# Performance work log

Measured on AMD Instinct MI355X. Metric: run time of the kernel, lower is better.

The kernel has to match this reference:

```python
import jax, jax.numpy as jnp
import numpy as np

BS, TPD, D = 16384, 4, 128
G, M = 4, 4096


def setup_inputs() -> dict:
    key = jax.random.key(0)
    k1, k2 = jax.random.split(key)
    return {
        "x": jax.random.normal(k1, (BS, TPD, D), dtype=jnp.float32),
        "embeddings": jax.random.normal(k2, (G, M, D), dtype=jnp.float32),
        "count": jnp.zeros((G, M), dtype=jnp.float32),
    }


def reference(x, embeddings, count):
    bs, tpd, d = x.shape
    g, m, _ = embeddings.shape
    # (BS, TPD, D) -> (N, G, D) -> (G, N, D), N = BS*TPD/G
    xg = x.reshape(-1, g, d).transpose(1, 0, 2)
    # squared euclidean distances (argmin identical to cdist argmin)
    x2 = jnp.sum(xg * xg, axis=-1)[:, :, None]            # (G, N, 1)
    e2 = jnp.sum(embeddings * embeddings, axis=-1)[:, None, :]  # (G, 1, M)
    dist = x2 + e2 - 2.0 * jnp.einsum('gnd,gmd->gnm', xg, embeddings)  # (G, N, M)
    indices = jnp.argmin(dist, axis=-1)                   # (G, N) int
    # usage-count scatter add (buffer update in torch forward)
    new_count = count.at[jnp.arange(g)[:, None], indices].add(1.0)
    # gather quantized embeddings: (G, N, D)
    x_quant = embeddings[jnp.arange(g)[:, None], indices]
    x_quant = x_quant.transpose(1, 0, 2).reshape(bs, tpd, d)
    ind_out = indices.transpose(1, 0).reshape(bs, tpd)
    return (x_quant, ind_out, new_count)
```

## Files before the change

kernel.cpp:

```cpp
#include <hip/hip_runtime.h>

#define G 4
#define M 4096
#define D 128
#define NQ 16384
#define NROWS 65536
#define OFF_IND 8388608
#define OFF_CNT (OFF_IND + NROWS)
#define DELTA 0.02f

typedef unsigned int u32;
typedef unsigned short u16;
typedef __attribute__((ext_vector_type(8))) short bf16x8;
typedef __attribute__((ext_vector_type(4))) float f32x4;

__device__ __forceinline__ u16 f2bf(float f) {
    u32 u = __float_as_uint(f);
    u32 r = (u + 0x7FFFu + ((u >> 16) & 1u)) >> 16;
    return (u16)r;
}
__device__ __forceinline__ float bf2f(u16 b) { return __uint_as_float((u32)b << 16); }


__global__ __launch_bounds__(256) void prep_x(const float* __restrict__ x,
                                              u32* __restrict__ xfrag) {
    const int tid = threadIdx.x, lane = tid & 63;
    const int c = blockIdx.x * 4 + (tid >> 6);
    const int ks = c & 3, qt = c >> 2;
    const int qrow = qt * 16 + (lane & 15);
    const int g = qrow >> 14, n = qrow & 16383;
    const int k = ks * 32 + (lane >> 4) * 8;
    const float* src = x + ((size_t)n * 4 + g) * D + k;
    const float4 a = *(const float4*)src;
    const float4 b = *(const float4*)(src + 4);
    const float v[8] = {a.x, a.y, a.z, a.w, b.x, b.y, b.z, b.w};
    u32 hi[4], lo[4];
#pragma unroll
    for (int i = 0; i < 4; ++i) {
        const float v0 = -2.0f * v[2 * i], v1 = -2.0f * v[2 * i + 1];
        const u16 h0 = f2bf(v0), h1 = f2bf(v1);
        const u16 l0 = f2bf(v0 - bf2f(h0)), l1 = f2bf(v1 - bf2f(h1));
        hi[i] = (u32)h0 | ((u32)h1 << 16);
        lo[i] = (u32)l0 | ((u32)l1 << 16);
    }
    const u32 base = (u32)((qt * 4 + ks) * 2) * 256 + lane * 4;
    *(uint4*)(xfrag + base)       = make_uint4(hi[0], hi[1], hi[2], hi[3]);
    *(uint4*)(xfrag + base + 256) = make_uint4(lo[0], lo[1], lo[2], lo[3]);
}

__global__ __launch_bounds__(256) void prep_emb(const float* __restrict__ emb,
                                                u32* __restrict__ efrag) {
    const int tid = threadIdx.x, lane = tid & 63;
    const int c = blockIdx.x * 4 + (tid >> 6);
    const int ks = c & 3, mt = (c >> 2) & 255, g = c >> 10;
    const int m = mt * 16 + (lane & 15);
    const int k = ks * 32 + (lane >> 4) * 8;
    const float* src = emb + ((size_t)g * M + m) * D + k;
    const float4 a = *(const float4*)src;
    const float4 b = *(const float4*)(src + 4);
    const float v[8] = {a.x, a.y, a.z, a.w, b.x, b.y, b.z, b.w};
    u32 hi[4], lo[4];
#pragma unroll
    for (int i = 0; i < 4; ++i) {
        const float v0 = v[2 * i], v1 = v[2 * i + 1];
        const u16 h0 = f2bf(v0), h1 = f2bf(v1);
        const u16 l0 = f2bf(v0 - bf2f(h0)), l1 = f2bf(v1 - bf2f(h1));
        hi[i] = (u32)h0 | ((u32)h1 << 16);
        lo[i] = (u32)l0 | ((u32)l1 << 16);
    }
    const u32 base = (u32)(g * 256 + mt) * 2048 + (u32)(ks * 2) * 256 + lane * 4;
    *(uint4*)(efrag + base)       = make_uint4(hi[0], hi[1], hi[2], hi[3]);
    *(uint4*)(efrag + base + 256) = make_uint4(lo[0], lo[1], lo[2], lo[3]);
}

__global__ __launch_bounds__(256) void e2f_kernel(const float* __restrict__ emb,
                                                  float* __restrict__ e2f) {
    const int row = blockIdx.x * 4 + (threadIdx.x >> 6);
    const int lane = threadIdx.x & 63;
    const float2 v = ((const float2*)(emb + (size_t)row * D))[lane];
    double s = (double)v.x * (double)v.x + (double)v.y * (double)v.y;
#pragma unroll
    for (int off = 1; off < 64; off <<= 1) s += __shfl_xor(s, off, 64);
    if (lane == 0) e2f[row] = (float)s;
}

__global__ __launch_bounds__(256) void vq_mfma(const u32* __restrict__ xfrag,
                                               const u32* __restrict__ efrag,
                                               const float* __restrict__ e2f,
                                               float* __restrict__ out,
                                               int* __restrict__ flagcnt,
                                               int* __restrict__ flaglist) {
    __shared__ float e2s[M];
    __shared__ u32 ebuf[2][2048];

    const int tid = threadIdx.x, w = tid >> 6, lane = tid & 63;
    const int g = blockIdx.x >> 7, qb = blockIdx.x & 127;

    const float* e2g = e2f + (size_t)g * M;
    for (int i = tid; i < M / 4; i += 256) ((float4*)e2s)[i] = ((const float4*)e2g)[i];

    const bf16x8* xp = (const bf16x8*)xfrag;
    const int qt0 = g * 1024 + qb * 8 + w * 2;
    bf16x8 xf[2][4][2];
#pragma unroll
    for (int f = 0; f < 2; ++f)
#pragma unroll
        for (int ks = 0; ks < 4; ++ks)
#pragma unroll
            for (int h = 0; h < 2; ++h)
                xf[f][ks][h] = xp[(size_t)(((qt0 + f) * 4 + ks) * 2 + h) * 64 + lane];

    float b1[8], b2[8];
    int i1[8];
#pragma unroll
    for (int s = 0; s < 8; ++s) { b1[s] = 3.4e38f; b2[s] = 3.4e38f; i1[s] = 0; }

    const uint4* eg = (const uint4*)(efrag + (size_t)g * 256 * 2048);
    {
        const uint4 s0 = eg[tid], s1 = eg[256 + tid];
        ((uint4*)ebuf[0])[tid] = s0;
        ((uint4*)ebuf[0])[256 + tid] = s1;
    }
    __syncthreads();

    int cur = 0;
    for (int mc = 0; mc < 256; ++mc) {
        uint4 s0, s1;
        const bool pf = (mc + 1 < 256);
        if (pf) {
            const uint4* src = eg + (size_t)(mc + 1) * 512;
            s0 = src[tid];
            s1 = src[256 + tid];
        }
        const bf16x8* bp = (const bf16x8*)ebuf[cur];
        bf16x8 bh[4], bl[4];
#pragma unroll
        for (int ks = 0; ks < 4; ++ks) {
            bh[ks] = bp[(ks * 2 + 0) * 64 + lane];
            bl[ks] = bp[(ks * 2 + 1) * 64 + lane];
        }
        f32x4 acc0 = {0.f, 0.f, 0.f, 0.f}, acc1 = {0.f, 0.f, 0.f, 0.f};
#pragma unroll
        for (int ks = 0; ks < 4; ++ks) {
            acc0 = __builtin_amdgcn_mfma_f32_16x16x32_bf16(xf[0][ks][1], bh[ks], acc0, 0, 0, 0);
            acc1 = __builtin_amdgcn_mfma_f32_16x16x32_bf16(xf[1][ks][1], bh[ks], acc1, 0, 0, 0);
        }
#pragma unroll
        for (int ks = 0; ks < 4; ++ks) {
            acc0 = __builtin_amdgcn_mfma_f32_16x16x32_bf16(xf[0][ks][0], bl[ks], acc0, 0, 0, 0);
            acc1 = __builtin_amdgcn_mfma_f32_16x16x32_bf16(xf[1][ks][0], bl[ks], acc1, 0, 0, 0);
        }
#pragma unroll
        for (int ks = 0; ks < 4; ++ks) {
            acc0 = __builtin_amdgcn_mfma_f32_16x16x32_bf16(xf[0][ks][0], bh[ks], acc0, 0, 0, 0);
            acc1 = __builtin_amdgcn_mfma_f32_16x16x32_bf16(xf[1][ks][0], bh[ks], acc1, 0, 0, 0);
        }
        const int mcol = mc * 16 + (lane & 15);
        const float e2m = e2s[mcol];
#pragma unroll
        for (int r = 0; r < 4; ++r) {
            const float s0v = acc0[r] + e2m;
            b2[r] = fminf(b2[r], fmaxf(b1[r], s0v));
            i1[r] = (s0v < b1[r]) ? mcol : i1[r];
            b1[r] = fminf(b1[r], s0v);
            const float s1v = acc1[r] + e2m;
            b2[r + 4] = fminf(b2[r + 4], fmaxf(b1[r + 4], s1v));
            i1[r + 4] = (s1v < b1[r + 4]) ? mcol : i1[r + 4];
            b1[r + 4] = fminf(b1[r + 4], s1v);
        }
        if (pf) {
            uint4* dst = (uint4*)ebuf[cur ^ 1];
            dst[tid] = s0;
            dst[256 + tid] = s1;
        }
        __syncthreads();
        cur ^= 1;
    }

#pragma unroll
    for (int s = 0; s < 8; ++s) {
        float v1 = b1[s], v2 = b2[s];
        int j1 = i1[s];
#pragma unroll
        for (int off = 1; off < 16; off <<= 1) {
            const float o1 = __shfl_xor(v1, off, 64);
            const int   oj = __shfl_xor(j1, off, 64);
            const float o2 = __shfl_xor(v2, off, 64);
            v2 = fminf(fminf(v2, o2), fmaxf(v1, o1));
            if (o1 < v1 || (o1 == v1 && oj < j1)) { v1 = o1; j1 = oj; }
        }
        if ((lane & 15) == 0) {
            const int n = qb * 128 + w * 32 + (s >> 2) * 16 + (lane >> 4) * 4 + (s & 3);
            if (v2 - v1 > DELTA) {
                out[(size_t)OFF_IND + (size_t)n * 4 + g] = (float)j1;
                atomicAdd(out + OFF_CNT + (size_t)g * M + j1, 1.0f);
            } else {
                const int pos = atomicAdd(flagcnt, 1);
                if (pos < NROWS) flaglist[pos] = (g << 14) | n;
            }
        }
    }
}

__global__ __launch_bounds__(256) void recheck(const float* __restrict__ x,
                                               const float* __restrict__ emb,
                                               const int* __restrict__ flagcnt,
                                               const int* __restrict__ flaglist,
                                               float* __restrict__ out) {
    __shared__ float xs[D];
    __shared__ double wv[4];
    __shared__ int wi[4];
    const int tid = threadIdx.x;
    int nf = *flagcnt;
    if (nf > NROWS) nf = NROWS;
    for (int it = blockIdx.x; it < nf; it += gridDim.x) {
        const int qid = flaglist[it];
        const int g = qid >> 14, n = qid & 16383;
        __syncthreads();
        if (tid < 32) ((float4*)xs)[tid] = ((const float4*)(x + ((size_t)n * 4 + g) * D))[tid];
        __syncthreads();
        double best = 1e300;
        int bi = 0;
        for (int j = 0; j < 16; ++j) {
            const int m = tid + j * 256;
            const float* e = emb + ((size_t)g * M + m) * D;
            double dot = 0.0, ee = 0.0;
            for (int k = 0; k < D; k += 4) {
                const float4 ev = *(const float4*)(e + k);
                const double e0 = ev.x, e1 = ev.y, e2v = ev.z, e3 = ev.w;
                dot = fma((double)xs[k + 0], e0, dot);
                dot = fma((double)xs[k + 1], e1, dot);
                dot = fma((double)xs[k + 2], e2v, dot);
                dot = fma((double)xs[k + 3], e3, dot);
                ee = fma(e0, e0, ee); ee = fma(e1, e1, ee);
                ee = fma(e2v, e2v, ee); ee = fma(e3, e3, ee);
            }
            const double s = ee - 2.0 * dot;
            if (s < best) { best = s; bi = m; }
        }
        for (int off = 1; off < 64; off <<= 1) {
            const double ob = __shfl_xor(best, off, 64);
            const int oi = __shfl_xor(bi, off, 64);
            if (ob < best || (ob == best && oi < bi)) { best = ob; bi = oi; }
        }
        if ((tid & 63) == 0) { wv[tid >> 6] = best; wi[tid >> 6] = bi; }
        __syncthreads();
        if (tid == 0) {
            double bv = wv[0];
            int bj = wi[0];
            for (int u = 1; u < 4; ++u)
                if (wv[u] < bv || (wv[u] == bv && wi[u] < bj)) { bv = wv[u]; bj = wi[u]; }
            out[(size_t)OFF_IND + (size_t)n * 4 + g] = (float)bj;
            atomicAdd(out + OFF_CNT + (size_t)g * M + bj, 1.0f);
        }
    }
}

__global__ __launch_bounds__(256) void gather_kernel(const float* __restrict__ emb,
                                                     const float* __restrict__ indf,
                                                     float* __restrict__ xq) {
    const int rid = blockIdx.x * 8 + (threadIdx.x >> 5);
    const int lane = threadIdx.x & 31;
    const int g = rid & 3;
    const int m = (int)indf[rid];
    const float4 v = ((const float4*)(emb + ((size_t)g * M + m) * D))[lane];
    ((float4*)(xq + (size_t)rid * D))[lane] = v;
}


#define QT 64
#define MT 128
#define KT 32
#define XPAD 132
#define EPAD 36

__global__ __launch_bounds__(256) void e2d_kernel(const float* __restrict__ emb,
                                                  double* __restrict__ e2) {
    int row = blockIdx.x * 4 + (threadIdx.x >> 6);
    int lane = threadIdx.x & 63;
    const float2 v = ((const float2*)(emb + (size_t)row * D))[lane];
    double s = (double)v.x * (double)v.x + (double)v.y * (double)v.y;
#pragma unroll
    for (int off = 1; off < 64; off <<= 1) s += __shfl_xor(s, off, 64);
    if (lane == 0) e2[row] = s;
}

__global__ __launch_bounds__(256) void argmin_kernel(const float* __restrict__ x,
                                                     const float* __restrict__ emb,
                                                     const double* __restrict__ e2,
                                                     float* __restrict__ out) {
    __shared__ float xs[QT][XPAD];
    __shared__ float es[MT][EPAD];
    const int g = blockIdx.x >> 8;
    const int n0 = (blockIdx.x & 255) * QT;
    const int tid = threadIdx.x;
    const int tm = tid & 15;
    const int tq = tid >> 4;
#pragma unroll
    for (int it = 0; it < 8; ++it) {
        int idx = it * 256 + tid;
        int r = idx >> 5, c2 = idx & 31;
        const float4 v = ((const float4*)(x + ((size_t)((n0 + r) * 4 + g)) * D))[c2];
        *(float4*)&xs[r][c2 * 4] = v;
    }
    double best[4];
    int bm[4];
#pragma unroll
    for (int qi = 0; qi < 4; ++qi) { best[qi] = 1e300; bm[qi] = 0; }
    const double* e2g = e2 + (size_t)g * M;
    const float* eg = emb + (size_t)g * M * D;
    for (int mc = 0; mc < M / MT; ++mc) {
        const int m0 = mc * MT;
        double acc[4][8];
#pragma unroll
        for (int qi = 0; qi < 4; ++qi)
#pragma unroll
            for (int mi = 0; mi < 8; ++mi) acc[qi][mi] = 0.0;
        for (int kc = 0; kc < D / KT; ++kc) {
            __syncthreads();
#pragma unroll
            for (int it = 0; it < 4; ++it) {
                int idx = it * 256 + tid;
                int r = idx >> 3, c2 = idx & 7;
                const float4 v = ((const float4*)(eg + (size_t)(m0 + r) * D + kc * KT))[c2];
                *(float4*)&es[r][c2 * 4] = v;
            }
            __syncthreads();
#pragma unroll
            for (int kk = 0; kk < KT; kk += 4) {
                double xv[4][4];
#pragma unroll
                for (int qi = 0; qi < 4; ++qi) {
                    const float4 v = *(const float4*)&xs[tq + 16 * qi][kc * KT + kk];
                    xv[qi][0] = v.x; xv[qi][1] = v.y; xv[qi][2] = v.z; xv[qi][3] = v.w;
                }
#pragma unroll
                for (int mi = 0; mi < 8; ++mi) {
                    const float4 v = *(const float4*)&es[tm + 16 * mi][kk];
                    const double e0 = v.x, e1 = v.y, e2v = v.z, e3 = v.w;
#pragma unroll
                    for (int qi = 0; qi < 4; ++qi) {
                        acc[qi][mi] = fma(xv[qi][0], e0, acc[qi][mi]);
                        acc[qi][mi] = fma(xv[qi][1], e1, acc[qi][mi]);
                        acc[qi][mi] = fma(xv[qi][2], e2v, acc[qi][mi]);
                        acc[qi][mi] = fma(xv[qi][3], e3, acc[qi][mi]);
                    }
                }
            }
        }
#pragma unroll
        for (int mi = 0; mi < 8; ++mi) {
            const int m = m0 + tm + 16 * mi;
            const double e2m = e2g[m];
#pragma unroll
            for (int qi = 0; qi < 4; ++qi) {
                const double s = e2m - 2.0 * acc[qi][mi];
                if (s < best[qi]) { best[qi] = s; bm[qi] = m; }
            }
        }
    }
#pragma unroll
    for (int qi = 0; qi < 4; ++qi) {
        double v = best[qi];
        int i = bm[qi];
#pragma unroll
        for (int off = 1; off < 16; off <<= 1) {
            const double ov = __shfl_xor(v, off, 64);
            const int oi = __shfl_xor(i, off, 64);
            if (ov < v || (ov == v && oi < i)) { v = ov; i = oi; }
        }
        if (tm == 0) {
            const int n = n0 + tq + 16 * qi;
            out[(size_t)OFF_IND + (size_t)n * 4 + g] = (float)i;
            atomicAdd(out + OFF_CNT + (size_t)g * M + i, 1.0f);
        }
    }
}


extern "C" void kernel_launch(void* const* d_in, const int* in_sizes, int n_in,
                              void* d_out, int out_size, void* d_ws, size_t ws_size,
                              hipStream_t stream) {
    const float* x   = (const float*)d_in[0];
    const float* emb = (const float*)d_in[1];
    const float* cnt = (const float*)d_in[2];
    float* out = (float*)d_out;

    if (ws_size >= 8716544) {
        u32*   efrag    = (u32*)d_ws;
        float* e2fp     = (float*)((char*)d_ws + 8388608);
        int*   flagcnt  = (int*)((char*)d_ws + 8454144);
        int*   flaglist = (int*)((char*)d_ws + 8454400);
        u32*   xfrag    = (u32*)d_out;

        hipLaunchKernelGGL(prep_x,   dim3(4096), dim3(256), 0, stream, x, xfrag);
        hipLaunchKernelGGL(prep_emb, dim3(1024), dim3(256), 0, stream, emb, efrag);
        hipLaunchKernelGGL(e2f_kernel, dim3(4096), dim3(256), 0, stream, emb, e2fp);
        hipMemcpyAsync(out + OFF_CNT, cnt, (size_t)G * M * sizeof(float),
                       hipMemcpyDeviceToDevice, stream);
        hipMemsetAsync(flagcnt, 0, 4, stream);
        hipLaunchKernelGGL(vq_mfma, dim3(512), dim3(256), 0, stream,
                           xfrag, efrag, e2fp, out, flagcnt, flaglist);
        hipLaunchKernelGGL(recheck, dim3(256), dim3(256), 0, stream,
                           x, emb, flagcnt, flaglist, out);
        hipLaunchKernelGGL(gather_kernel, dim3(NROWS / 8), dim3(256), 0, stream,
                           emb, out + OFF_IND, out);
    } else {
        double* e2 = (double*)d_ws;
        hipLaunchKernelGGL(e2d_kernel, dim3(4096), dim3(256), 0, stream, emb, e2);
        hipMemcpyAsync(out + OFF_CNT, cnt, (size_t)G * M * sizeof(float),
                       hipMemcpyDeviceToDevice, stream);
        hipLaunchKernelGGL(argmin_kernel, dim3((NQ / QT) * G), dim3(256), 0, stream,
                           x, emb, e2, out);
        hipLaunchKernelGGL(gather_kernel, dim3(NROWS / 8), dim3(256), 0, stream,
                           emb, out + OFF_IND, out);
    }
}
```

Baseline: 368.4 us.

## Split codebook across blocks, fuse x prep into MFMA kernel, merge partial argmins

The main distance kernel now splits each group's codebook into two halves, which doubles the grid to 1024 blocks for better CU occupancy. A new merge kernel combines the per-half best and second-best results before the ambiguity check. The x bf16 hi/lo conversion moves into the MFMA kernel, and the embedding-norm computation is fused into the embedding prep kernel with atomics. The e2 bias is folded into the MFMA accumulator init, and the recheck grid is enlarged. This adds partial-result traffic and a launch, and the norms are now accumulated in float instead of double.

```diff
diff --git a/kernel.cpp b/kernel.cpp
--- a/kernel.cpp
+++ b/kernel.cpp
@@ -16,40 +16,16 @@
 
 __device__ __forceinline__ u16 f2bf(float f) {
     u32 u = __float_as_uint(f);
-    u32 r = (u + 0x7FFFu + ((u >> 16) & 1u)) >> 16;
-    return (u16)r;
+    return (u16)((u + 0x7FFFu + ((u >> 16) & 1u)) >> 16);
 }
 __device__ __forceinline__ float bf2f(u16 b) { return __uint_as_float((u32)b << 16); }
 
-
-__global__ __launch_bounds__(256) void prep_x(const float* __restrict__ x,
-                                              u32* __restrict__ xfrag) {
-    const int tid = threadIdx.x, lane = tid & 63;
-    const int c = blockIdx.x * 4 + (tid >> 6);
-    const int ks = c & 3, qt = c >> 2;
-    const int qrow = qt * 16 + (lane & 15);
-    const int g = qrow >> 14, n = qrow & 16383;
-    const int k = ks * 32 + (lane >> 4) * 8;
-    const float* src = x + ((size_t)n * 4 + g) * D + k;
-    const float4 a = *(const float4*)src;
-    const float4 b = *(const float4*)(src + 4);
-    const float v[8] = {a.x, a.y, a.z, a.w, b.x, b.y, b.z, b.w};
-    u32 hi[4], lo[4];
-#pragma unroll
-    for (int i = 0; i < 4; ++i) {
-        const float v0 = -2.0f * v[2 * i], v1 = -2.0f * v[2 * i + 1];
-        const u16 h0 = f2bf(v0), h1 = f2bf(v1);
-        const u16 l0 = f2bf(v0 - bf2f(h0)), l1 = f2bf(v1 - bf2f(h1));
-        hi[i] = (u32)h0 | ((u32)h1 << 16);
-        lo[i] = (u32)l0 | ((u32)l1 << 16);
-    }
-    const u32 base = (u32)((qt * 4 + ks) * 2) * 256 + lane * 4;
-    *(uint4*)(xfrag + base)       = make_uint4(hi[0], hi[1], hi[2], hi[3]);
-    *(uint4*)(xfrag + base + 256) = make_uint4(lo[0], lo[1], lo[2], lo[3]);
-}
-
-__global__ __launch_bounds__(256) void prep_emb(const float* __restrict__ emb,
-                                                u32* __restrict__ efrag) {
+union bfpack { bf16x8 v; u32 u[4]; };
+
+
+__global__ __launch_bounds__(256) void prep_emb_e2(const float* __restrict__ emb,
+                                                   u32* __restrict__ efrag,
+                                                   float* __restrict__ e2f) {
     const int tid = threadIdx.x, lane = tid & 63;
     const int c = blockIdx.x * 4 + (tid >> 6);
     const int ks = c & 3, mt = (c >> 2) & 255, g = c >> 10;
@@ -59,6 +35,9 @@
     const float4 a = *(const float4*)src;
     const float4 b = *(const float4*)(src + 4);
     const float v[8] = {a.x, a.y, a.z, a.w, b.x, b.y, b.z, b.w};
+    float ss = 0.f;
+#pragma unroll
+    for (int i = 0; i < 8; ++i) ss = fmaf(v[i], v[i], ss);
     u32 hi[4], lo[4];
 #pragma unroll
     for (int i = 0; i < 4; ++i) {
@@ -71,51 +50,60 @@
     const u32 base = (u32)(g * 256 + mt) * 2048 + (u32)(ks * 2) * 256 + lane * 4;
     *(uint4*)(efrag + base)       = make_uint4(hi[0], hi[1], hi[2], hi[3]);
     *(uint4*)(efrag + base + 256) = make_uint4(lo[0], lo[1], lo[2], lo[3]);
-}
-
-__global__ __launch_bounds__(256) void e2f_kernel(const float* __restrict__ emb,
-                                                  float* __restrict__ e2f) {
-    const int row = blockIdx.x * 4 + (threadIdx.x >> 6);
-    const int lane = threadIdx.x & 63;
-    const float2 v = ((const float2*)(emb + (size_t)row * D))[lane];
-    double s = (double)v.x * (double)v.x + (double)v.y * (double)v.y;
-#pragma unroll
-    for (int off = 1; off < 64; off <<= 1) s += __shfl_xor(s, off, 64);
-    if (lane == 0) e2f[row] = (float)s;
-}
-
-__global__ __launch_bounds__(256) void vq_mfma(const u32* __restrict__ xfrag,
-                                               const u32* __restrict__ efrag,
-                                               const float* __restrict__ e2f,
-                                               float* __restrict__ out,
-                                               int* __restrict__ flagcnt,
-                                               int* __restrict__ flaglist) {
-    __shared__ float e2s[M];
+    ss += __shfl_xor(ss, 16, 64);
+    ss += __shfl_xor(ss, 32, 64);
+    if (lane < 16) atomicAdd(&e2f[g * M + m], ss);
+}
+
+__global__ __launch_bounds__(256) void vq_mfma2(const float* __restrict__ x,
+                                                const u32* __restrict__ efrag,
+                                                const float* __restrict__ e2f,
+                                                float* __restrict__ pb1,
+                                                float* __restrict__ pb2,
+                                                int* __restrict__ pi1) {
+    __shared__ float e2s[2048];
     __shared__ u32 ebuf[2][2048];
 
     const int tid = threadIdx.x, w = tid >> 6, lane = tid & 63;
-    const int g = blockIdx.x >> 7, qb = blockIdx.x & 127;
-
-    const float* e2g = e2f + (size_t)g * M;
-    for (int i = tid; i < M / 4; i += 256) ((float4*)e2s)[i] = ((const float4*)e2g)[i];
-
-    const bf16x8* xp = (const bf16x8*)xfrag;
-    const int qt0 = g * 1024 + qb * 8 + w * 2;
+    const int combo = blockIdx.x & 7;
+    const int g = combo >> 1, half = combo & 1;
+    const int qb = blockIdx.x >> 3;
+
+    const float* e2g = e2f + (size_t)g * M + half * 2048;
+    for (int i = tid; i < 512; i += 256) ((float4*)e2s)[i] = ((const float4*)e2g)[i];
+
+    const int qt0 = qb * 8 + w * 2;
     bf16x8 xf[2][4][2];
 #pragma unroll
-    for (int f = 0; f < 2; ++f)
-#pragma unroll
-        for (int ks = 0; ks < 4; ++ks)
-#pragma unroll
-            for (int h = 0; h < 2; ++h)
-                xf[f][ks][h] = xp[(size_t)(((qt0 + f) * 4 + ks) * 2 + h) * 64 + lane];
+    for (int f = 0; f < 2; ++f) {
+        const int n = (qt0 + f) * 16 + (lane & 15);
+#pragma unroll
+        for (int ks = 0; ks < 4; ++ks) {
+            const int k = ks * 32 + (lane >> 4) * 8;
+            const float* src = x + ((size_t)n * 4 + g) * D + k;
+            const float4 a = *(const float4*)src;
+            const float4 b = *(const float4*)(src + 4);
+            const float v[8] = {a.x, a.y, a.z, a.w, b.x, b.y, b.z, b.w};
+            bfpack ph, pl;
+#pragma unroll
+            for (int i = 0; i < 4; ++i) {
+                const float v0 = -2.0f * v[2 * i], v1 = -2.0f * v[2 * i + 1];
+                const u16 h0 = f2bf(v0), h1 = f2bf(v1);
+                const u16 l0 = f2bf(v0 - bf2f(h0)), l1 = f2bf(v1 - bf2f(h1));
+                ph.u[i] = (u32)h0 | ((u32)h1 << 16);
+                pl.u[i] = (u32)l0 | ((u32)l1 << 16);
+            }
+            xf[f][ks][0] = ph.v;
+            xf[f][ks][1] = pl.v;
+        }
+    }
 
     float b1[8], b2[8];
     int i1[8];
 #pragma unroll
     for (int s = 0; s < 8; ++s) { b1[s] = 3.4e38f; b2[s] = 3.4e38f; i1[s] = 0; }
 
-    const uint4* eg = (const uint4*)(efrag + (size_t)g * 256 * 2048);
+    const uint4* eg = (const uint4*)(efrag + (size_t)(g * 256 + half * 128) * 2048);
     {
         const uint4 s0 = eg[tid], s1 = eg[256 + tid];
         ((uint4*)ebuf[0])[tid] = s0;
@@ -124,9 +112,10 @@
     __syncthreads();
 
     int cur = 0;
-    for (int mc = 0; mc < 256; ++mc) {
+    const int mb0 = half * 2048;
+    for (int mc = 0; mc < 128; ++mc) {
         uint4 s0, s1;
-        const bool pf = (mc + 1 < 256);
+        const bool pf = (mc + 1 < 128);
         if (pf) {
             const uint4* src = eg + (size_t)(mc + 1) * 512;
             s0 = src[tid];
@@ -139,9 +128,14 @@
             bh[ks] = bp[(ks * 2 + 0) * 64 + lane];
             bl[ks] = bp[(ks * 2 + 1) * 64 + lane];
         }
-        f32x4 acc0 = {0.f, 0.f, 0.f, 0.f}, acc1 = {0.f, 0.f, 0.f, 0.f};
-#pragma unroll
-        for (int ks = 0; ks < 4; ++ks) {
+        const int mcol = mb0 + mc * 16 + (lane & 15);
+        const float e2c = e2s[mc * 16 + (lane & 15)];
+        const f32x4 init = {e2c, e2c, e2c, e2c};
+        f32x4 acc0, acc1;
+        acc0 = __builtin_amdgcn_mfma_f32_16x16x32_bf16(xf[0][0][1], bh[0], init, 0, 0, 0);
+        acc1 = __builtin_amdgcn_mfma_f32_16x16x32_bf16(xf[1][0][1], bh[0], init, 0, 0, 0);
+#pragma unroll
+        for (int ks = 1; ks < 4; ++ks) {
             acc0 = __builtin_amdgcn_mfma_f32_16x16x32_bf16(xf[0][ks][1], bh[ks], acc0, 0, 0, 0);
             acc1 = __builtin_amdgcn_mfma_f32_16x16x32_bf16(xf[1][ks][1], bh[ks], acc1, 0, 0, 0);
         }
@@ -155,15 +149,13 @@
             acc0 = __builtin_amdgcn_mfma_f32_16x16x32_bf16(xf[0][ks][0], bh[ks], acc0, 0, 0, 0);
             acc1 = __builtin_amdgcn_mfma_f32_16x16x32_bf16(xf[1][ks][0], bh[ks], acc1, 0, 0, 0);
         }
-        const int mcol = mc * 16 + (lane & 15);
-        const float e2m = e2s[mcol];
 #pragma unroll
         for (int r = 0; r < 4; ++r) {
-            const float s0v = acc0[r] + e2m;
+            const float s0v = acc0[r];
             b2[r] = fminf(b2[r], fmaxf(b1[r], s0v));
             i1[r] = (s0v < b1[r]) ? mcol : i1[r];
             b1[r] = fminf(b1[r], s0v);
-            const float s1v = acc1[r] + e2m;
+            const float s1v = acc1[r];
             b2[r + 4] = fminf(b2[r + 4], fmaxf(b1[r + 4], s1v));
             i1[r + 4] = (s1v < b1[r + 4]) ? mcol : i1[r + 4];
             b1[r + 4] = fminf(b1[r + 4], s1v);
@@ -190,15 +182,35 @@
             if (o1 < v1 || (o1 == v1 && oj < j1)) { v1 = o1; j1 = oj; }
         }
         if ((lane & 15) == 0) {
-            const int n = qb * 128 + w * 32 + (s >> 2) * 16 + (lane >> 4) * 4 + (s & 3);
-            if (v2 - v1 > DELTA) {
-                out[(size_t)OFF_IND + (size_t)n * 4 + g] = (float)j1;
-                atomicAdd(out + OFF_CNT + (size_t)g * M + j1, 1.0f);
-            } else {
-                const int pos = atomicAdd(flagcnt, 1);
-                if (pos < NROWS) flaglist[pos] = (g << 14) | n;
-            }
-        }
+            const int n = (qt0 + (s >> 2)) * 16 + (lane >> 4) * 4 + (s & 3);
+            const int pidx = ((((g << 14) | n)) << 1) | half;
+            pb1[pidx] = v1;
+            pb2[pidx] = v2;
+            pi1[pidx] = j1;
+        }
+    }
+}
+
+__global__ __launch_bounds__(256) void merge_kernel(const float* __restrict__ pb1,
+                                                    const float* __restrict__ pb2,
+                                                    const int* __restrict__ pi1,
+                                                    float* __restrict__ out,
+                                                    int* __restrict__ flagcnt,
+                                                    int* __restrict__ flaglist) {
+    const int t = blockIdx.x * 256 + threadIdx.x;
+    const float v1a = pb1[2 * t], v1b = pb1[2 * t + 1];
+    const float v2a = pb2[2 * t], v2b = pb2[2 * t + 1];
+    const int   ia = pi1[2 * t],  ib = pi1[2 * t + 1];
+    const float v1 = fminf(v1a, v1b);
+    const int   i  = (v1b < v1a) ? ib : ia;
+    const float v2 = fminf(fminf(v2a, v2b), fmaxf(v1a, v1b));
+    const int g = t >> 14, n = t & 16383;
+    if (v2 - v1 > DELTA) {
+        out[(size_t)OFF_IND + (size_t)n * 4 + g] = (float)i;
+        atomicAdd(out + OFF_CNT + (size_t)g * M + i, 1.0f);
+    } else {
+        const int pos = atomicAdd(flagcnt, 1);
+        flaglist[pos] = t;
     }
 }
 
@@ -391,17 +403,19 @@
         float* e2fp     = (float*)((char*)d_ws + 8388608);
         int*   flagcnt  = (int*)((char*)d_ws + 8454144);
         int*   flaglist = (int*)((char*)d_ws + 8454400);
-        u32*   xfrag    = (u32*)d_out;
-
-        hipLaunchKernelGGL(prep_x,   dim3(4096), dim3(256), 0, stream, x, xfrag);
-        hipLaunchKernelGGL(prep_emb, dim3(1024), dim3(256), 0, stream, emb, efrag);
-        hipLaunchKernelGGL(e2f_kernel, dim3(4096), dim3(256), 0, stream, emb, e2fp);
+        float* pb1 = out;
+        float* pb2 = out + 131072;
+        int*   pi1 = (int*)(out + 262144);
+
+        hipMemsetAsync((char*)d_ws + 8388608, 0, 65792, stream);
+        hipLaunchKernelGGL(prep_emb_e2, dim3(1024), dim3(256), 0, stream, emb, efrag, e2fp);
         hipMemcpyAsync(out + OFF_CNT, cnt, (size_t)G * M * sizeof(float),
                        hipMemcpyDeviceToDevice, stream);
-        hipMemsetAsync(flagcnt, 0, 4, stream);
-        hipLaunchKernelGGL(vq_mfma, dim3(512), dim3(256), 0, stream,
-                           xfrag, efrag, e2fp, out, flagcnt, flaglist);
-        hipLaunchKernelGGL(recheck, dim3(256), dim3(256), 0, stream,
+        hipLaunchKernelGGL(vq_mfma2, dim3(1024), dim3(256), 0, stream,
+                           x, efrag, e2fp, pb1, pb2, pi1);
+        hipLaunchKernelGGL(merge_kernel, dim3(256), dim3(256), 0, stream,
+                           pb1, pb2, pi1, out, flagcnt, flaglist);
+        hipLaunchKernelGGL(recheck, dim3(2048), dim3(256), 0, stream,
                            x, emb, flagcnt, flaglist, out);
         hipLaunchKernelGGL(gather_kernel, dim3(NROWS / 8), dim3(256), 0, stream,
                            emb, out + OFF_IND, out);
```

New measurement: 356.7 us. -3.2%, faster.
